# Optimization experiments

Measured on AMD Instinct MI355X. Metric: run time of the kernel, lower is better.

## Reference

```python
import jax, jax.numpy as jnp
import numpy as np


def _rope(xh, theta_factor):
    # xh: [H, S, Dqk]; rotate first half against second half (as in source)
    S, D = xh.shape[-2], xh.shape[-1]
    d_rope = D // 2
    rate = theta_factor * (-jnp.arange(0, d_rope, dtype=xh.dtype) / d_rope)
    pos = jnp.arange(0, S, dtype=xh.dtype)
    rot = pos[:, None] * rate[None, :]            # [S, d_rope]
    sin, cos = jnp.sin(rot), jnp.cos(rot)
    x1, x2 = xh[..., :d_rope], xh[..., d_rope:]
    y1 = cos * x1 - sin * x2
    y2 = sin * x1 + cos * x2
    return jnp.concatenate([y1, y2], axis=-1)


def _mha(x, y, q, k, v, o, theta_factor):
    S = x.shape[0]
    d_model = x.shape[1]
    x_scale = 1.0 / jnp.sqrt(jnp.array(x.shape[1], x.dtype))
    y_scale = 1.0 / jnp.sqrt(jnp.array(y.shape[1], x.dtype))
    # causal additive mask: 0 on/below diagonal, -1e9 above
    mask = (jnp.tril(jnp.ones((S, S), x.dtype)) - 1.0) * 1000000000.0
    # per-head projections (note: source uses x_scale for both q and k)
    pre_q = jnp.einsum('sd,hdk->hsk', x, q) * x_scale
    pre_k = jnp.einsum('td,hdk->htk', y, k) * x_scale
    vs = jnp.einsum('td,hdv->htv', y, v) * y_scale
    rq = _rope(pre_q, theta_factor)
    rk = _rope(pre_k, theta_factor)
    attn_scale = 1.0 / jnp.sqrt(jnp.array(rq.shape[-1], x.dtype))
    scores = jnp.einsum('hsk,htk->hst', rq, rk) * attn_scale + mask
    w = jax.nn.softmax(scores, axis=-1)           # [H, S, S]
    z = jnp.einsum('hst,htv->hsv', w, vs)         # [H, S, Dv]
    out_scale = 1.0 / jnp.sqrt(jnp.array(o.shape[0] * o.shape[1], x.dtype))
    return jnp.einsum('hsv,hvd->sd', z, o) * out_scale


def setup_inputs() -> dict:
    key = jax.random.key(0)
    ks = jax.random.split(key, 5)
    S, D, H, Dqk, Dv = 2048, 2048, 16, 128, 128
    return {
        'x': jax.random.normal(ks[0], (S, D), jnp.float32),
        'q': jax.random.normal(ks[1], (H, D, Dqk), jnp.float32),
        'k': jax.random.normal(ks[2], (H, D, Dqk), jnp.float32),
        'v': jax.random.normal(ks[3], (H, D, Dv), jnp.float32),
        'o': jax.random.normal(ks[4], (H, Dv, D), jnp.float32),
        'theta_factor': jnp.array(10000.0, jnp.float32),
    }


def reference(x, q, k, v, o, theta_factor):
    # self-attention path (y = x), scale = 1
    return _mha(x, x, q, k, v, o, theta_factor)
```

## Files before the change

### kernel.cpp

```cpp
#include <hip/hip_runtime.h>


#define S_LEN   2048
#define D_MODEL 2048
#define NHEAD   16
#define DHEAD   128

using f32x4   = __attribute__((ext_vector_type(4))) float;
using f32x16  = __attribute__((ext_vector_type(16))) float;
using bf16x8  = __attribute__((ext_vector_type(8))) __bf16;

__device__ __forceinline__ unsigned short f2bf(float f) {
  unsigned int u = __builtin_bit_cast(unsigned int, f);
  u += 0x7fffu + ((u >> 16) & 1u);
  return (unsigned short)(u >> 16);
}
__device__ __forceinline__ int chunks_of(int qt) { return (4 * qt + 13) / 10; }

__device__ __forceinline__ void gl_lds16(const unsigned short* g, char* l) {
  __builtin_amdgcn_global_load_lds(
      (const __attribute__((address_space(1))) unsigned int*)g,
      (__attribute__((address_space(3))) unsigned int*)l, 16, 0, 0);
}

__global__ __launch_bounds__(256) void k_prep(
    const float* __restrict__ x, const float* __restrict__ q,
    const float* __restrict__ k, const float* __restrict__ v,
    const float* __restrict__ o, const float* __restrict__ theta_p,
    unsigned short* __restrict__ xb, unsigned short* __restrict__ wT,
    unsigned short* __restrict__ obT, float* __restrict__ sint,
    float* __restrict__ cost) {
  __shared__ float t[32][33];
  const int bid = blockIdx.x, tid = threadIdx.x;
  if (bid < 4096) {
    int i = (bid * 256 + tid) * 4;
    float4 vv = *reinterpret_cast<const float4*>(x + i);
    ushort4 ov; ov.x = f2bf(vv.x); ov.y = f2bf(vv.y); ov.z = f2bf(vv.z); ov.w = f2bf(vv.w);
    *reinterpret_cast<ushort4*>(xb + i) = ov;
  } else if (bid < 4608) {
    int i = (bid - 4096) * 256 + tid;
    int s = i >> 6, c = i & 63;
    float rate = theta_p[0] * (-(float)c / 64.0f);
    float sn, cs;
    sincosf((float)s * rate, &sn, &cs);
    sint[i] = sn; cost[i] = cs;
  } else {
    int ti = bid - 4608;
    int which = ti >> 12, i = ti & 4095;
    const float* ip; unsigned short* op; int C, b, rt, ct;
    const int R = 2048;
    if (which < 3) {
      C = 128; b = i >> 8; rt = (i >> 2) & 63; ct = i & 3;
      const float* src = which == 0 ? q : (which == 1 ? k : v);
      ip = src + (size_t)b * R * C;
      op = wT + (size_t)which * 4194304 + (size_t)b * R * C;
    } else {
      C = 2048; rt = i >> 6; ct = i & 63;
      ip = o; op = obT;
    }
    int tx = tid & 31, ty = tid >> 5;
    #pragma unroll
    for (int j = 0; j < 4; j++)
      t[ty + j * 8][tx] = ip[(size_t)(rt * 32 + ty + j * 8) * C + ct * 32 + tx];
    __syncthreads();
    #pragma unroll
    for (int j = 0; j < 4; j++)
      op[(size_t)(ct * 32 + ty + j * 8) * R + rt * 32 + tx] = f2bf(t[tx][ty + j * 8]);
  }
}

__global__ __launch_bounds__(256) void k_proj2(
    const unsigned short* __restrict__ xb, const unsigned short* __restrict__ wT,
    const float* __restrict__ sint, const float* __restrict__ cost,
    unsigned short* __restrict__ rq, unsigned short* __restrict__ rk,
    unsigned short* __restrict__ vst) {
  __shared__ char lds[65536];
  const int tid = threadIdx.x, l = tid & 63, w = tid >> 6;
  const int lr = l & 15, lk = l >> 4;
  const int orig = blockIdx.x;
  const int wg = (orig & 7) * 96 + (orig >> 3);
  const int bx = wg & 15, by = wg >> 4;
  const int s0 = bx * 128;
  const int h = by & 15, which = by >> 4;
  const unsigned short* bbase = wT + (size_t)by * 128 * D_MODEL;

  f32x4 acc[2][8] = {};

  auto stage = [&](int t, int buf) {
    const int kt = t * 64;
    char* dst = lds + buf * 32768;
    #pragma unroll
    for (int j = 0; j < 4; j++) {
      int ci = (j * 4 + w) * 64 + l;
      int r = ci >> 3, c8 = ci & 7;
      int csrc = (c8 ^ (r & 7)) * 8;
      gl_lds16(xb + (size_t)(s0 + r) * D_MODEL + kt + csrc, dst + ci * 16);
      gl_lds16(bbase + (size_t)r * D_MODEL + kt + csrc, dst + 16384 + ci * 16);
    }
  };

  stage(0, 0);
  int cur = 0;
  const int nT = D_MODEL / 64;
  for (int t = 0; t < nT; t++) {
    if (t + 1 < nT) {
      stage(t + 1, cur ^ 1);
      asm volatile("s_waitcnt vmcnt(8)" ::: "memory");
    } else {
      asm volatile("s_waitcnt vmcnt(0)" ::: "memory");
    }
    __builtin_amdgcn_s_barrier();
    const char* base = lds + cur * 32768;
    #pragma unroll
    for (int kk = 0; kk < 2; kk++) {
      const int kb = kk * 64 + lk * 16;
      bf16x8 a[2], b[8];
      #pragma unroll
      for (int mf = 0; mf < 2; mf++) {
        int rr = w * 32 + mf * 16 + lr;
        a[mf] = *reinterpret_cast<const bf16x8*>(base + rr * 128 + (kb ^ ((rr & 7) << 4)));
      }
      #pragma unroll
      for (int nf = 0; nf < 8; nf++) {
        int rn = nf * 16 + lr;
        b[nf] = *reinterpret_cast<const bf16x8*>(base + 16384 + rn * 128 + (kb ^ ((rn & 7) << 4)));
      }
      #pragma unroll
      for (int mf = 0; mf < 2; mf++)
        #pragma unroll
        for (int nf = 0; nf < 8; nf++)
          acc[mf][nf] = __builtin_amdgcn_mfma_f32_16x16x32_bf16(a[mf], b[nf], acc[mf][nf], 0, 0, 0);
    }
    asm volatile("s_waitcnt lgkmcnt(0)" ::: "memory");
    __builtin_amdgcn_s_barrier();
    cur ^= 1;
  }

  const float xscale = 0.022097086912079608f;
  const float qsc = xscale * 0.08838834764831845f;
  if (which < 2) {
    const float sc_out = (which == 0) ? qsc : xscale;
    unsigned short* dst = (which == 0 ? rq : rk) + (size_t)h * S_LEN * DHEAD;
    #pragma unroll
    for (int mf = 0; mf < 2; mf++) {
      #pragma unroll
      for (int nf = 0; nf < 4; nf++) {
        int c1 = nf * 16 + lr;
        #pragma unroll
        for (int rg = 0; rg < 4; rg++) {
          int srow = s0 + w * 32 + mf * 16 + lk * 4 + rg;
          float sn = sint[srow * 64 + c1], cs = cost[srow * 64 + c1];
          float x1 = acc[mf][nf][rg] * sc_out;
          float x2 = acc[mf][nf + 4][rg] * sc_out;
          dst[(size_t)srow * DHEAD + c1]      = f2bf(cs * x1 - sn * x2);
          dst[(size_t)srow * DHEAD + c1 + 64] = f2bf(sn * x1 + cs * x2);
        }
      }
    }
  } else {
    unsigned short* dst = vst + (size_t)h * DHEAD * S_LEN;
    #pragma unroll
    for (int mf = 0; mf < 2; mf++) {
      int rbase = s0 + w * 32 + mf * 16 + lk * 4;
      #pragma unroll
      for (int nf = 0; nf < 8; nf++) {
        int c = nf * 16 + lr;
        ushort4 ov;
        ov.x = f2bf(acc[mf][nf][0] * xscale); ov.y = f2bf(acc[mf][nf][1] * xscale);
        ov.z = f2bf(acc[mf][nf][2] * xscale); ov.w = f2bf(acc[mf][nf][3] * xscale);
        *reinterpret_cast<ushort4*>(dst + (size_t)c * S_LEN + rbase) = ov;
      }
    }
  }
}

__global__ __launch_bounds__(256, 2) void k_attn6(
    const unsigned short* __restrict__ rq, const unsigned short* __restrict__ rk,
    const unsigned short* __restrict__ vst,
    unsigned short* __restrict__ opart, float2* __restrict__ mlbuf) {
  __shared__ uint4 ldsbuf[2368];
  char* lds = (char*)ldsbuf;
  const int tid = threadIdx.x, l = tid & 63, w = tid >> 6;
  const int hi = l >> 5, qcol = l & 31;
  const int b = blockIdx.x;
  const int h = b & 15;
  int u = b >> 4, qt = 0;
  while (u >= chunks_of(qt)) { u -= chunks_of(qt); qt++; }
  const int ntile = 4 * qt + 4;
  const int tbeg = u * 10;
  const int tend = (tbeg + 10 < ntile) ? tbeg + 10 : ntile;
  const int s0w = qt * 128 + w * 32;
  const int wlast = s0w + 31;
  const int dtile = s0w >> 5;

  const unsigned short* rk_h  = rk  + (size_t)h * S_LEN * DHEAD;
  const unsigned short* vst_h = vst + (size_t)h * DHEAD * S_LEN;

  const unsigned short* qrow_p = rq + ((size_t)h * S_LEN + s0w + qcol) * DHEAD + hi * 8;
  bf16x8 qb[8];
  #pragma unroll
  for (int kk = 0; kk < 8; kk++)
    qb[kk] = *reinterpret_cast<const bf16x8*>(qrow_p + kk * 16);

  f32x16 O[4] = {};
  float mrow = -3.0e38f, lrow = 0.0f;

  uint4 kreg[2], vreg[2];
  auto ld_regs = [&](int t) {
    const int t0 = t * 32;
    #pragma unroll
    for (int j = 0; j < 2; j++) {
      int ci = tid + j * 256;
      kreg[j] = *reinterpret_cast<const uint4*>(rk_h + (size_t)(t0 + (ci >> 4)) * DHEAD + (ci & 15) * 8);
      vreg[j] = *reinterpret_cast<const uint4*>(vst_h + (size_t)(ci >> 2) * S_LEN + t0 + (ci & 3) * 8);
    }
  };
  auto wr_lds = [&](int p) {
    char* dst = lds + p * 18944;
    #pragma unroll
    for (int j = 0; j < 2; j++) {
      int ci = tid + j * 256;
      *reinterpret_cast<uint4*>(dst + (ci >> 4) * 272 + (ci & 15) * 16) = kreg[j];
      *reinterpret_cast<uint4*>(dst + 8704 + (ci >> 2) * 80 + (ci & 3) * 16) = vreg[j];
    }
  };

  ld_regs(tbeg);
  wr_lds(0);
  if (tbeg + 1 < tend) ld_regs(tbeg + 1);
  asm volatile("s_waitcnt lgkmcnt(0)" ::: "memory");
  __builtin_amdgcn_s_barrier();

  int cur = 0;
  for (int t = tbeg; t < tend; t++) {
    const char* kb = lds + cur * 18944;
    const char* vb = kb + 8704;
    const int tt0 = t * 32;
    if (tt0 <= wlast) {
      f32x16 sc = {};
      __builtin_amdgcn_s_setprio(1);
      #pragma unroll
      for (int kk = 0; kk < 8; kk++) {
        bf16x8 ka = *reinterpret_cast<const bf16x8*>(kb + qcol * 272 + kk * 32 + hi * 16);
        sc = __builtin_amdgcn_mfma_f32_32x32x16_bf16(ka, qb[kk], sc, 0, 0, 0);
      }
      __builtin_amdgcn_s_setprio(0);
      float p[16];
      #pragma unroll
      for (int r = 0; r < 16; r++) p[r] = sc[r];
      if (t == dtile) {
        #pragma unroll
        for (int r = 0; r < 16; r++)
          if (((r & 3) + 8 * (r >> 2) + 4 * hi) > qcol) p[r] = -1.0e9f;
      }
      float mx[8];
      #pragma unroll
      for (int i = 0; i < 8; i++) mx[i] = fmaxf(p[2 * i], p[2 * i + 1]);
      #pragma unroll
      for (int i = 0; i < 4; i++) mx[i] = fmaxf(mx[i], mx[i + 4]);
      mx[0] = fmaxf(mx[0], mx[2]); mx[1] = fmaxf(mx[1], mx[3]);
      float pmax = fmaxf(mx[0], mx[1]);
      pmax = fmaxf(pmax, __shfl_xor(pmax, 32, 64));
      if (__any(pmax > mrow + 8.0f)) {
        float mn = fmaxf(mrow, pmax);
        float sf = __expf(mrow - mn);
        lrow *= sf; mrow = mn;
        #pragma unroll
        for (int vc = 0; vc < 4; vc++)
          #pragma unroll
          for (int r = 0; r < 16; r++) O[vc][r] *= sf;
      }
      #pragma unroll
      for (int r = 0; r < 16; r++) p[r] = __expf(p[r] - mrow);
      float sm[8];
      #pragma unroll
      for (int i = 0; i < 8; i++) sm[i] = p[2 * i] + p[2 * i + 1];
      #pragma unroll
      for (int i = 0; i < 4; i++) sm[i] += sm[i + 4];
      float psum = (sm[0] + sm[1]) + (sm[2] + sm[3]);
      psum += __shfl_xor(psum, 32, 64);
      lrow += psum;
      unsigned int pk[2][4], sw[2][4];
      #pragma unroll
      for (int c = 0; c < 2; c++)
        #pragma unroll
        for (int k = 0; k < 4; k++) {
          unsigned int r_;
          asm("v_cvt_pk_bf16_f32 %0, %1, %2" : "=v"(r_)
              : "v"(p[8 * c + 2 * k]), "v"(p[8 * c + 2 * k + 1]));
          pk[c][k] = r_;
          sw[c][k] = (unsigned int)__shfl_xor((int)r_, 32, 64);
        }
      bf16x8 pb[2];
      #pragma unroll
      for (int c = 0; c < 2; c++) {
        union { unsigned int u4[4]; bf16x8 v; } bw;
        bw.u4[0] = hi ? sw[c][2] : pk[c][0];
        bw.u4[1] = hi ? sw[c][3] : pk[c][1];
        bw.u4[2] = hi ? pk[c][2] : sw[c][0];
        bw.u4[3] = hi ? pk[c][3] : sw[c][1];
        pb[c] = bw.v;
      }
      __builtin_amdgcn_s_setprio(1);
      #pragma unroll
      for (int vc = 0; vc < 4; vc++) {
        const char* vrow = vb + (vc * 32 + qcol) * 80 + hi * 16;
        bf16x8 va0 = *reinterpret_cast<const bf16x8*>(vrow);
        bf16x8 va1 = *reinterpret_cast<const bf16x8*>(vrow + 32);
        O[vc] = __builtin_amdgcn_mfma_f32_32x32x16_bf16(va0, pb[0], O[vc], 0, 0, 0);
        O[vc] = __builtin_amdgcn_mfma_f32_32x32x16_bf16(va1, pb[1], O[vc], 0, 0, 0);
      }
      __builtin_amdgcn_s_setprio(0);
    }
    if (t + 1 < tend) {
      wr_lds(cur ^ 1);
      if (t + 2 < tend) ld_regs(t + 2);
    }
    asm volatile("s_waitcnt lgkmcnt(0)" ::: "memory");
    __builtin_amdgcn_s_barrier();
    cur ^= 1;
  }

  float inv = lrow > 0.0f ? 1.0f / lrow : 0.0f;
  #pragma unroll
  for (int vc = 0; vc < 4; vc++)
    #pragma unroll
    for (int g = 0; g < 4; g++) {
      int v0 = vc * 32 + 8 * g + 4 * hi;
      ushort4 ov;
      ov.x = f2bf(O[vc][4 * g + 0] * inv); ov.y = f2bf(O[vc][4 * g + 1] * inv);
      ov.z = f2bf(O[vc][4 * g + 2] * inv); ov.w = f2bf(O[vc][4 * g + 3] * inv);
      *reinterpret_cast<ushort4*>(lds + (w * 32 + qcol) * 272 + v0 * 2) = ov;
    }
  __syncthreads();
  #pragma unroll
  for (int j = 0; j < 8; j++) {
    int row = w * 32 + j * 4 + (l >> 4);
    uint4 vv = *reinterpret_cast<const uint4*>(lds + row * 272 + (l & 15) * 16);
    *reinterpret_cast<uint4*>(opart + ((size_t)b * 128 + row) * DHEAD + (l & 15) * 8) = vv;
  }
  if (l < 32)
    mlbuf[(size_t)b * 128 + w * 32 + l] = make_float2(mrow, lrow);
}

__global__ void k_comb2(const unsigned short* __restrict__ opart,
                        const float2* __restrict__ mlbuf,
                        unsigned short* __restrict__ z) {
  int g = blockIdx.x * 256 + threadIdx.x;
  int vg = g & 15, q = (g >> 4) & 2047, h = g >> 15;
  int qt = q >> 7, r = q & 127;
  int base = 0;
  for (int j = 0; j < qt; j++) base += chunks_of(j);
  const int nc = chunks_of(qt);
  float m = -3.0e38f;
  float2 ml[7];
  #pragma unroll
  for (int cc = 0; cc < 7; cc++)
    if (cc < nc) {
      ml[cc] = mlbuf[(size_t)((base + cc) * 16 + h) * 128 + r];
      m = fmaxf(m, ml[cc].x);
    }
  float wts[7], wsum = 0.0f;
  #pragma unroll
  for (int cc = 0; cc < 7; cc++)
    if (cc < nc) {
      float wv = ml[cc].y > 0.0f ? ml[cc].y * __expf(ml[cc].x - m) : 0.0f;
      wts[cc] = wv; wsum += wv;
    }
  float wi = 1.0f / wsum;
  float acc[8] = {};
  #pragma unroll
  for (int cc = 0; cc < 7; cc++)
    if (cc < nc && wts[cc] > 0.0f) {
      float wv = wts[cc] * wi;
      bf16x8 v = *reinterpret_cast<const bf16x8*>(
          opart + ((size_t)((base + cc) * 16 + h) * 128 + r) * DHEAD + vg * 8);
      #pragma unroll
      for (int j = 0; j < 8; j++) acc[j] += wv * (float)v[j];
    }
  unsigned short* zp = z + (size_t)q * D_MODEL + h * DHEAD + vg * 8;
  ushort4 lo, hi4;
  lo.x = f2bf(acc[0]); lo.y = f2bf(acc[1]); lo.z = f2bf(acc[2]); lo.w = f2bf(acc[3]);
  hi4.x = f2bf(acc[4]); hi4.y = f2bf(acc[5]); hi4.z = f2bf(acc[6]); hi4.w = f2bf(acc[7]);
  *reinterpret_cast<ushort4*>(zp) = lo;
  *reinterpret_cast<ushort4*>(zp + 4) = hi4;
}

__global__ __launch_bounds__(256) void k_out2(
    const unsigned short* __restrict__ zb, const unsigned short* __restrict__ obT,
    float* __restrict__ out) {
  __shared__ char lds[49152];
  const int tid = threadIdx.x, l = tid & 63, w = tid >> 6;
  const int lr = l & 15, lk = l >> 4;
  const int orig = blockIdx.x;
  const int wg = (orig & 7) * 64 + (orig >> 3);
  const int bx = wg & 31, by = wg >> 5;
  const int s0 = bx * 64, n0 = by * 128;
  const int wm = w >> 1, wn = w & 1;
  f32x4 acc[2][4] = {};

  auto stage = [&](int t, int buf) {
    const int kt = t * 64;
    char* dst = lds + buf * 24576;
    #pragma unroll
    for (int j = 0; j < 2; j++) {
      int ci = tid + j * 256;
      int r = ci >> 3, c8 = ci & 7;
      int csrc = (c8 ^ (r & 7)) * 8;
      gl_lds16(zb + (size_t)(s0 + r) * D_MODEL + kt + csrc, dst + ci * 16);
    }
    #pragma unroll
    for (int j = 0; j < 4; j++) {
      int ci = tid + j * 256;
      int r = ci >> 3, c8 = ci & 7;
      int csrc = (c8 ^ (r & 7)) * 8;
      gl_lds16(obT + (size_t)(n0 + r) * D_MODEL + kt + csrc, dst + 8192 + ci * 16);
    }
  };

  stage(0, 0);
  int cur = 0;
  const int nT = D_MODEL / 64;
  for (int t = 0; t < nT; t++) {
    if (t + 1 < nT) {
      stage(t + 1, cur ^ 1);
      asm volatile("s_waitcnt vmcnt(6)" ::: "memory");
    } else {
      asm volatile("s_waitcnt vmcnt(0)" ::: "memory");
    }
    __builtin_amdgcn_s_barrier();
    const char* base = lds + cur * 24576;
    #pragma unroll
    for (int kk = 0; kk < 2; kk++) {
      const int kb = kk * 64 + lk * 16;
      bf16x8 a[2], b[4];
      #pragma unroll
      for (int mf = 0; mf < 2; mf++) {
        int rr = wm * 32 + mf * 16 + lr;
        a[mf] = *reinterpret_cast<const bf16x8*>(base + rr * 128 + (kb ^ ((rr & 7) << 4)));
      }
      #pragma unroll
      for (int nf = 0; nf < 4; nf++) {
        int rn = wn * 64 + nf * 16 + lr;
        b[nf] = *reinterpret_cast<const bf16x8*>(base + 8192 + rn * 128 + (kb ^ ((rn & 7) << 4)));
      }
      #pragma unroll
      for (int mf = 0; mf < 2; mf++)
        #pragma unroll
        for (int nf = 0; nf < 4; nf++)
          acc[mf][nf] = __builtin_amdgcn_mfma_f32_16x16x32_bf16(a[mf], b[nf], acc[mf][nf], 0, 0, 0);
    }
    asm volatile("s_waitcnt lgkmcnt(0)" ::: "memory");
    __builtin_amdgcn_s_barrier();
    cur ^= 1;
  }
  const float osc = 0.022097086912079608f;
  #pragma unroll
  for (int mf = 0; mf < 2; mf++)
    #pragma unroll
    for (int nf = 0; nf < 4; nf++)
      #pragma unroll
      for (int rg = 0; rg < 4; rg++)
        out[(size_t)(s0 + wm * 32 + mf * 16 + lk * 4 + rg) * D_MODEL + n0 + wn * 64 + nf * 16 + lr]
            = acc[mf][nf][rg] * osc;
}

extern "C" void kernel_launch(void* const* d_in, const int* in_sizes, int n_in,
                              void* d_out, int out_size, void* d_ws, size_t ws_size,
                              hipStream_t stream) {
  const float* x = (const float*)d_in[0];
  const float* q = (const float*)d_in[1];
  const float* k = (const float*)d_in[2];
  const float* v = (const float*)d_in[3];
  const float* o = (const float*)d_in[4];
  const float* theta = (const float*)d_in[5];
  float* out = (float*)d_out;

  char* ws = (char*)d_ws;
  const size_t MB = 1u << 20;
  unsigned short* xb  = (unsigned short*)(ws + 0 * MB);
  unsigned short* qbT = (unsigned short*)(ws + 8 * MB);
  unsigned short* obT = (unsigned short*)(ws + 32 * MB);
  unsigned short* rq  = (unsigned short*)(ws + 40 * MB);
  unsigned short* rk  = (unsigned short*)(ws + 48 * MB);
  unsigned short* vst = (unsigned short*)(ws + 56 * MB);
  float* sint = (float*)(ws + 64 * MB);
  float* cost = (float*)(ws + 64 * MB + 512 * 1024);
  unsigned short* opart = (unsigned short*)(ws + 0 * MB);
  float2* mlbuf         = (float2*)(ws + 31 * MB);
  unsigned short* zb    = (unsigned short*)(ws + 40 * MB);

  k_prep<<<dim3(20992), dim3(256), 0, stream>>>(x, q, k, v, o, theta, xb, qbT, obT, sint, cost);
  k_proj2<<<dim3(768), dim3(256), 0, stream>>>(xb, qbT, sint, cost, rq, rk, vst);
  k_attn6<<<dim3(976), dim3(256), 0, stream>>>(rq, rk, vst, opart, mlbuf);
  k_comb2<<<dim3(2048), dim3(256), 0, stream>>>(opart, mlbuf, zb);
  k_out2<<<dim3(512), dim3(256), 0, stream>>>(zb, obT, out);
}
```

Baseline: 173.3 us.

## Give each wave private K/V LDS staging and drop block barriers in attention

Each of the four waves in the attention kernel now loads its own K and V tiles into a private LDS region and walks only the key tiles it needs, up to its own diagonal tile. This removes the per-tile block-wide barriers and stops waves past the causal boundary from sitting idle at barriers. In exchange, each block fetches the same K/V tiles four times from global/L2 memory, and the LDS footprint grows to about 74 KB per block. The output staging also uses the per-wave region, so the final __syncthreads goes away.

```diff
diff --git a/kernel.cpp b/kernel.cpp
--- a/kernel.cpp
+++ b/kernel.cpp
@@ -174,12 +174,11 @@
   }
 }
 
-__global__ __launch_bounds__(256, 2) void k_attn6(
+__global__ __launch_bounds__(256, 2) void k_attn8(
     const unsigned short* __restrict__ rq, const unsigned short* __restrict__ rk,
     const unsigned short* __restrict__ vst,
     unsigned short* __restrict__ opart, float2* __restrict__ mlbuf) {
-  __shared__ uint4 ldsbuf[2368];
-  char* lds = (char*)ldsbuf;
+  __shared__ char lds[75776];
   const int tid = threadIdx.x, l = tid & 63, w = tid >> 6;
   const int hi = l >> 5, qcol = l & 31;
   const int b = blockIdx.x;
@@ -190,8 +189,11 @@
   const int tbeg = u * 10;
   const int tend = (tbeg + 10 < ntile) ? tbeg + 10 : ntile;
   const int s0w = qt * 128 + w * 32;
-  const int wlast = s0w + 31;
   const int dtile = s0w >> 5;
+  const int wend = (tend < dtile + 1) ? tend : dtile + 1;
+
+  char* kb = lds + w * 18944;
+  char* vb = kb + 8704;
 
   const unsigned short* rk_h  = rk  + (size_t)h * S_LEN * DHEAD;
   const unsigned short* vst_h = vst + (size_t)h * DHEAD * S_LEN;
@@ -205,120 +207,112 @@
   f32x16 O[4] = {};
   float mrow = -3.0e38f, lrow = 0.0f;
 
-  uint4 kreg[2], vreg[2];
+  uint4 kreg[8], vreg[8];
   auto ld_regs = [&](int t) {
     const int t0 = t * 32;
     #pragma unroll
-    for (int j = 0; j < 2; j++) {
-      int ci = tid + j * 256;
-      kreg[j] = *reinterpret_cast<const uint4*>(rk_h + (size_t)(t0 + (ci >> 4)) * DHEAD + (ci & 15) * 8);
-      vreg[j] = *reinterpret_cast<const uint4*>(vst_h + (size_t)(ci >> 2) * S_LEN + t0 + (ci & 3) * 8);
+    for (int j = 0; j < 8; j++) {
+      int ci = j * 64 + l;
+      kreg[j] = *reinterpret_cast<const uint4*>(
+          rk_h + (size_t)(t0 + (ci >> 4)) * DHEAD + (ci & 15) * 8);
+      vreg[j] = *reinterpret_cast<const uint4*>(
+          vst_h + (size_t)(ci >> 2) * S_LEN + t0 + (ci & 3) * 8);
     }
   };
-  auto wr_lds = [&](int p) {
-    char* dst = lds + p * 18944;
-    #pragma unroll
-    for (int j = 0; j < 2; j++) {
-      int ci = tid + j * 256;
-      *reinterpret_cast<uint4*>(dst + (ci >> 4) * 272 + (ci & 15) * 16) = kreg[j];
-      *reinterpret_cast<uint4*>(dst + 8704 + (ci >> 2) * 80 + (ci & 3) * 16) = vreg[j];
+  auto wr_lds = [&]() {
+    #pragma unroll
+    for (int j = 0; j < 8; j++) {
+      int ci = j * 64 + l;
+      *reinterpret_cast<uint4*>(kb + (ci >> 4) * 272 + (ci & 15) * 16) = kreg[j];
+      *reinterpret_cast<uint4*>(vb + (ci >> 2) * 80 + (ci & 3) * 16) = vreg[j];
     }
   };
 
-  ld_regs(tbeg);
-  wr_lds(0);
-  if (tbeg + 1 < tend) ld_regs(tbeg + 1);
-  asm volatile("s_waitcnt lgkmcnt(0)" ::: "memory");
-  __builtin_amdgcn_s_barrier();
-
-  int cur = 0;
-  for (int t = tbeg; t < tend; t++) {
-    const char* kb = lds + cur * 18944;
-    const char* vb = kb + 8704;
-    const int tt0 = t * 32;
-    if (tt0 <= wlast) {
-      f32x16 sc = {};
-      __builtin_amdgcn_s_setprio(1);
-      #pragma unroll
-      for (int kk = 0; kk < 8; kk++) {
-        bf16x8 ka = *reinterpret_cast<const bf16x8*>(kb + qcol * 272 + kk * 32 + hi * 16);
-        sc = __builtin_amdgcn_mfma_f32_32x32x16_bf16(ka, qb[kk], sc, 0, 0, 0);
-      }
-      __builtin_amdgcn_s_setprio(0);
-      float p[16];
-      #pragma unroll
-      for (int r = 0; r < 16; r++) p[r] = sc[r];
-      if (t == dtile) {
+  if (tbeg < wend) {
+    ld_regs(tbeg);
+    wr_lds();
+    if (tbeg + 1 < wend) ld_regs(tbeg + 1);
+  }
+
+  for (int t = tbeg; t < wend; t++) {
+    f32x16 sc = {};
+    __builtin_amdgcn_s_setprio(1);
+    #pragma unroll
+    for (int kk = 0; kk < 8; kk++) {
+      bf16x8 ka = *reinterpret_cast<const bf16x8*>(kb + qcol * 272 + kk * 32 + hi * 16);
+      sc = __builtin_amdgcn_mfma_f32_32x32x16_bf16(ka, qb[kk], sc, 0, 0, 0);
+    }
+    __builtin_amdgcn_s_setprio(0);
+    float p[16];
+    #pragma unroll
+    for (int r = 0; r < 16; r++) p[r] = sc[r];
+    if (t == dtile) {
+      #pragma unroll
+      for (int r = 0; r < 16; r++)
+        if (((r & 3) + 8 * (r >> 2) + 4 * hi) > qcol) p[r] = -1.0e9f;
+    }
+    float mx[8];
+    #pragma unroll
+    for (int i = 0; i < 8; i++) mx[i] = fmaxf(p[2 * i], p[2 * i + 1]);
+    #pragma unroll
+    for (int i = 0; i < 4; i++) mx[i] = fmaxf(mx[i], mx[i + 4]);
+    mx[0] = fmaxf(mx[0], mx[2]); mx[1] = fmaxf(mx[1], mx[3]);
+    float pmax = fmaxf(mx[0], mx[1]);
+    pmax = fmaxf(pmax, __shfl_xor(pmax, 32, 64));
+    if (__any(pmax > mrow + 8.0f)) {
+      float mn = fmaxf(mrow, pmax);
+      float sf = __expf(mrow - mn);
+      lrow *= sf; mrow = mn;
+      #pragma unroll
+      for (int vc = 0; vc < 4; vc++)
         #pragma unroll
-        for (int r = 0; r < 16; r++)
-          if (((r & 3) + 8 * (r >> 2) + 4 * hi) > qcol) p[r] = -1.0e9f;
-      }
-      float mx[8];
-      #pragma unroll
-      for (int i = 0; i < 8; i++) mx[i] = fmaxf(p[2 * i], p[2 * i + 1]);
-      #pragma unroll
-      for (int i = 0; i < 4; i++) mx[i] = fmaxf(mx[i], mx[i + 4]);
-      mx[0] = fmaxf(mx[0], mx[2]); mx[1] = fmaxf(mx[1], mx[3]);
-      float pmax = fmaxf(mx[0], mx[1]);
-      pmax = fmaxf(pmax, __shfl_xor(pmax, 32, 64));
-      if (__any(pmax > mrow + 8.0f)) {
-        float mn = fmaxf(mrow, pmax);
-        float sf = __expf(mrow - mn);
-        lrow *= sf; mrow = mn;
-        #pragma unroll
-        for (int vc = 0; vc < 4; vc++)
-          #pragma unroll
-          for (int r = 0; r < 16; r++) O[vc][r] *= sf;
-      }
-      #pragma unroll
-      for (int r = 0; r < 16; r++) p[r] = __expf(p[r] - mrow);
-      float sm[8];
-      #pragma unroll
-      for (int i = 0; i < 8; i++) sm[i] = p[2 * i] + p[2 * i + 1];
-      #pragma unroll
-      for (int i = 0; i < 4; i++) sm[i] += sm[i + 4];
-      float psum = (sm[0] + sm[1]) + (sm[2] + sm[3]);
-      psum += __shfl_xor(psum, 32, 64);
-      lrow += psum;
-      unsigned int pk[2][4], sw[2][4];
-      #pragma unroll
-      for (int c = 0; c < 2; c++)
-        #pragma unroll
-        for (int k = 0; k < 4; k++) {
-          unsigned int r_;
-          asm("v_cvt_pk_bf16_f32 %0, %1, %2" : "=v"(r_)
-              : "v"(p[8 * c + 2 * k]), "v"(p[8 * c + 2 * k + 1]));
-          pk[c][k] = r_;
-          sw[c][k] = (unsigned int)__shfl_xor((int)r_, 32, 64);
-        }
-      bf16x8 pb[2];
-      #pragma unroll
-      for (int c = 0; c < 2; c++) {
-        union { unsigned int u4[4]; bf16x8 v; } bw;
-        bw.u4[0] = hi ? sw[c][2] : pk[c][0];
-        bw.u4[1] = hi ? sw[c][3] : pk[c][1];
-        bw.u4[2] = hi ? pk[c][2] : sw[c][0];
-        bw.u4[3] = hi ? pk[c][3] : sw[c][1];
-        pb[c] = bw.v;
-      }
-      __builtin_amdgcn_s_setprio(1);
-      #pragma unroll
-      for (int vc = 0; vc < 4; vc++) {
-        const char* vrow = vb + (vc * 32 + qcol) * 80 + hi * 16;
-        bf16x8 va0 = *reinterpret_cast<const bf16x8*>(vrow);
-        bf16x8 va1 = *reinterpret_cast<const bf16x8*>(vrow + 32);
-        O[vc] = __builtin_amdgcn_mfma_f32_32x32x16_bf16(va0, pb[0], O[vc], 0, 0, 0);
-        O[vc] = __builtin_amdgcn_mfma_f32_32x32x16_bf16(va1, pb[1], O[vc], 0, 0, 0);
-      }
-      __builtin_amdgcn_s_setprio(0);
-    }
-    if (t + 1 < tend) {
-      wr_lds(cur ^ 1);
-      if (t + 2 < tend) ld_regs(t + 2);
-    }
-    asm volatile("s_waitcnt lgkmcnt(0)" ::: "memory");
-    __builtin_amdgcn_s_barrier();
-    cur ^= 1;
+        for (int r = 0; r < 16; r++) O[vc][r] *= sf;
+    }
+    #pragma unroll
+    for (int r = 0; r < 16; r++) p[r] = __expf(p[r] - mrow);
+    float sm[8];
+    #pragma unroll
+    for (int i = 0; i < 8; i++) sm[i] = p[2 * i] + p[2 * i + 1];
+    #pragma unroll
+    for (int i = 0; i < 4; i++) sm[i] += sm[i + 4];
+    float psum = (sm[0] + sm[1]) + (sm[2] + sm[3]);
+    psum += __shfl_xor(psum, 32, 64);
+    lrow += psum;
+    unsigned int pk[2][4], sw[2][4];
+    #pragma unroll
+    for (int c = 0; c < 2; c++)
+      #pragma unroll
+      for (int k = 0; k < 4; k++) {
+        unsigned int r_;
+        asm("v_cvt_pk_bf16_f32 %0, %1, %2" : "=v"(r_)
+            : "v"(p[8 * c + 2 * k]), "v"(p[8 * c + 2 * k + 1]));
+        pk[c][k] = r_;
+        sw[c][k] = (unsigned int)__shfl_xor((int)r_, 32, 64);
+      }
+    bf16x8 pb[2];
+    #pragma unroll
+    for (int c = 0; c < 2; c++) {
+      union { unsigned int u4[4]; bf16x8 v; } bw;
+      bw.u4[0] = hi ? sw[c][2] : pk[c][0];
+      bw.u4[1] = hi ? sw[c][3] : pk[c][1];
+      bw.u4[2] = hi ? pk[c][2] : sw[c][0];
+      bw.u4[3] = hi ? pk[c][3] : sw[c][1];
+      pb[c] = bw.v;
+    }
+    __builtin_amdgcn_s_setprio(1);
+    #pragma unroll
+    for (int vc = 0; vc < 4; vc++) {
+      const char* vrow = vb + (vc * 32 + qcol) * 80 + hi * 16;
+      bf16x8 va0 = *reinterpret_cast<const bf16x8*>(vrow);
+      bf16x8 va1 = *reinterpret_cast<const bf16x8*>(vrow + 32);
+      O[vc] = __builtin_amdgcn_mfma_f32_32x32x16_bf16(va0, pb[0], O[vc], 0, 0, 0);
+      O[vc] = __builtin_amdgcn_mfma_f32_32x32x16_bf16(va1, pb[1], O[vc], 0, 0, 0);
+    }
+    __builtin_amdgcn_s_setprio(0);
+    if (t + 1 < wend) {
+      wr_lds();
+      if (t + 2 < wend) ld_regs(t + 2);
+    }
   }
 
   float inv = lrow > 0.0f ? 1.0f / lrow : 0.0f;
@@ -330,14 +324,13 @@
       ushort4 ov;
       ov.x = f2bf(O[vc][4 * g + 0] * inv); ov.y = f2bf(O[vc][4 * g + 1] * inv);
       ov.z = f2bf(O[vc][4 * g + 2] * inv); ov.w = f2bf(O[vc][4 * g + 3] * inv);
-      *reinterpret_cast<ushort4*>(lds + (w * 32 + qcol) * 272 + v0 * 2) = ov;
-    }
-  __syncthreads();
+      *reinterpret_cast<ushort4*>(kb + qcol * 272 + v0 * 2) = ov;
+    }
   #pragma unroll
   for (int j = 0; j < 8; j++) {
-    int row = w * 32 + j * 4 + (l >> 4);
-    uint4 vv = *reinterpret_cast<const uint4*>(lds + row * 272 + (l & 15) * 16);
-    *reinterpret_cast<uint4*>(opart + ((size_t)b * 128 + row) * DHEAD + (l & 15) * 8) = vv;
+    int lr8 = j * 4 + (l >> 4);
+    uint4 vv = *reinterpret_cast<const uint4*>(kb + lr8 * 272 + (l & 15) * 16);
+    *reinterpret_cast<uint4*>(opart + ((size_t)b * 128 + w * 32 + lr8) * DHEAD + (l & 15) * 8) = vv;
   }
   if (l < 32)
     mlbuf[(size_t)b * 128 + w * 32 + l] = make_float2(mrow, lrow);
@@ -492,7 +485,7 @@
 
   k_prep<<<dim3(20992), dim3(256), 0, stream>>>(x, q, k, v, o, theta, xb, qbT, obT, sint, cost);
   k_proj2<<<dim3(768), dim3(256), 0, stream>>>(xb, qbT, sint, cost, rq, rk, vst);
-  k_attn6<<<dim3(976), dim3(256), 0, stream>>>(rq, rk, vst, opart, mlbuf);
+  k_attn8<<<dim3(976), dim3(256), 0, stream>>>(rq, rk, vst, opart, mlbuf);
   k_comb2<<<dim3(2048), dim3(256), 0, stream>>>(opart, mlbuf, zb);
   k_out2<<<dim3(512), dim3(256), 0, stream>>>(zb, obT, out);
 }
```

Result: slower. 284.4 us (+64.1%).
